# Optimization experiments

Measured on AMD Instinct MI355X. Metric: run time of the kernel, lower is better.

## Reference

```python
import jax, jax.numpy as jnp
import numpy as np
from jax.scipy.special import erfc

# Constants baked into PmeModule.__init__ (NNPOps PME)
GRID = (14, 15, 16)          # reciprocal mesh
ORDER = 5                    # B-spline order
ALPHA = 4.985823141035867    # Ewald splitting parameter (1/nm)
COULOMB = 138.935            # ONE_4PI_EPS0, kJ/mol*nm/e^2
CUTOFF = 0.5                 # direct-space cutoff (forward arg in source)
N_ATOMS = 4096


def _M(k, x):
    """Cardinal B-spline M_k evaluated elementwise (Essmann et al. 1995)."""
    if k == 1:
        return jnp.where((x >= 0.0) & (x < 1.0), 1.0, 0.0)
    return (x * _M(k - 1, x) + (k - x) * _M(k - 1, x - 1.0)) / (k - 1)


def _bspline_moduli(K):
    """|b(m)|^2 per axis; zero out ill-defined modes (odd order, m=K/2)."""
    m = jnp.arange(K)
    kk = jnp.arange(ORDER - 1, dtype=jnp.float32)
    Mv = _M(ORDER, kk + 1.0)                                   # M_n(1..n-1)
    ph = jnp.exp(2j * jnp.pi * m[:, None] * kk[None, :] / K)
    denom = (Mv[None, :] * ph).sum(-1)
    d2 = jnp.abs(denom) ** 2
    return jnp.where(d2 < 1e-7, 0.0, 1.0 / d2)


def _direct(positions, charges, box):
    # All-pairs minimum-image (triclinic-reduced) erfc/r sum within cutoff.
    delta = positions[:, None, :] - positions[None, :, :]      # [N,N,3]
    for a in (2, 1, 0):
        delta = delta - box[a] * jnp.round(delta[..., a:a + 1] / box[a, a])
    r2 = (delta ** 2).sum(-1)                                  # [N,N]
    n = positions.shape[0]
    mask = (r2 < CUTOFF ** 2) & ~jnp.eye(n, dtype=bool)
    r = jnp.sqrt(jnp.where(mask, r2, 1.0))
    qq = charges[:, None] * charges[None, :]
    e = jnp.where(mask, qq * erfc(ALPHA * r) / r, 0.0)
    return 0.5 * COULOMB * e.sum()                             # each pair once


def _spread(positions, charges, box):
    """Spread charges onto the mesh with order-5 B-splines (periodic)."""
    frac = positions @ jnp.linalg.inv(box)                     # fractional coords
    frac = frac - jnp.floor(frac)                              # wrap to [0,1)
    u = frac * jnp.array(GRID, jnp.float32)                    # [N,3]
    base = jnp.floor(u)
    w = u - base
    offs = jnp.arange(ORDER, dtype=jnp.float32)
    wts = _M(ORDER, w[:, :, None] + offs[None, None, :])       # [N,3,ORDER]
    idx = (base.astype(jnp.int32)[:, :, None]
           - jnp.arange(ORDER, dtype=jnp.int32)[None, None, :]) \
          % jnp.array(GRID, jnp.int32)[None, :, None]          # [N,3,ORDER]
    wq = (charges[:, None, None, None] * wts[:, 0, :, None, None]
          * wts[:, 1, None, :, None] * wts[:, 2, None, None, :])  # [N,5,5,5]
    fi = (idx[:, 0, :, None, None] * (GRID[1] * GRID[2])
          + idx[:, 1, None, :, None] * GRID[2]
          + idx[:, 2, None, None, :])                          # flat indices
    g = jnp.zeros(GRID[0] * GRID[1] * GRID[2], positions.dtype)
    return g.at[fi.reshape(-1)].add(wq.reshape(-1)).reshape(GRID)


def _reciprocal(positions, charges, box):
    Q = _spread(positions, charges, box)
    F = jnp.fft.fftn(Q)
    recip = jnp.linalg.inv(box)                                # recip vecs = columns
    mx = jnp.fft.fftfreq(GRID[0]) * GRID[0]
    my = jnp.fft.fftfreq(GRID[1]) * GRID[1]
    mz = jnp.fft.fftfreq(GRID[2]) * GRID[2]
    mv = (mx[:, None, None, None] * recip.T[0]
          + my[None, :, None, None] * recip.T[1]
          + mz[None, None, :, None] * recip.T[2])              # [Kx,Ky,Kz,3]
    m2 = (mv ** 2).sum(-1)
    B = (_bspline_moduli(GRID[0])[:, None, None]
         * _bspline_moduli(GRID[1])[None, :, None]
         * _bspline_moduli(GRID[2])[None, None, :])
    nz = m2 > 0.0
    m2s = jnp.where(nz, m2, 1.0)
    green = jnp.where(nz, jnp.exp(-(jnp.pi ** 2) * m2s / ALPHA ** 2) / m2s, 0.0)
    V = jnp.abs(jnp.linalg.det(box))
    erec = COULOMB / (2.0 * jnp.pi * V) * (green * B * jnp.abs(F) ** 2).sum()
    eself = -COULOMB * ALPHA / jnp.sqrt(jnp.pi) * (charges ** 2).sum()
    return erec + eself


def setup_inputs() -> dict:
    key = jax.random.key(0)
    k1, k2 = jax.random.split(key)
    box = jnp.diag(jnp.array([3.0, 3.1, 3.2], jnp.float32))    # nm, diagonal box
    positions = jax.random.uniform(k1, (N_ATOMS, 3), jnp.float32) * jnp.diag(box)
    charges = 0.5 * jax.random.normal(k2, (N_ATOMS,), jnp.float32)
    return {"positions": positions, "charges": charges, "box_vectors": box}


def reference(positions, charges, box_vectors):
    edir = _direct(positions, charges, box_vectors)
    erecip = _reciprocal(positions, charges, box_vectors)
    return edir - erecip
```

## Files before the change

### kernel.cpp

```cpp
#include <hip/hip_runtime.h>
#include <math.h>

#define NATOM 4096
#define KX 14
#define KY 15
#define KZ 16
#define SLAB (KY*KZ)
#define NGRID (KX*SLAB)
#define NB 128
#define APB (NATOM/NB)
#define NTRI 544

static constexpr float ALPHA_F   = 4.985823141035867f;
static constexpr float COULOMB_F = 138.935f;
static constexpr float CUT2_F    = 0.25f;
static constexpr float TWOPI_F   = 6.283185307179586f;
static constexpr float PI_F      = 3.14159265358979f;

#define POIS32 0xAAAAAAAAu
#define CTR_LAST (POIS32 + 15u)

__device__ __forceinline__ float M1f(float x){ return (x >= 0.f && x < 1.f) ? 1.f : 0.f; }
__device__ __forceinline__ float M2f(float x){ return x*M1f(x) + (2.f-x)*M1f(x-1.f); }
__device__ __forceinline__ float M3f(float x){ return (x*M2f(x) + (3.f-x)*M2f(x-1.f)) * 0.5f; }
__device__ __forceinline__ float M4f(float x){ return (x*M3f(x) + (4.f-x)*M3f(x-1.f)) * (1.f/3.f); }
__device__ __forceinline__ float M5f(float x){ return (x*M4f(x) + (5.f-x)*M4f(x-1.f)) * 0.25f; }

__device__ __forceinline__ void inv3x3(const float* b, float* inv){
  float det = b[0]*(b[4]*b[8]-b[5]*b[7]) - b[1]*(b[3]*b[8]-b[5]*b[6]) + b[2]*(b[3]*b[7]-b[4]*b[6]);
  float id = 1.f/det;
  inv[0] = (b[4]*b[8]-b[5]*b[7])*id;
  inv[1] = (b[2]*b[7]-b[1]*b[8])*id;
  inv[2] = (b[1]*b[5]-b[2]*b[4])*id;
  inv[3] = (b[5]*b[6]-b[3]*b[8])*id;
  inv[4] = (b[0]*b[8]-b[2]*b[6])*id;
  inv[5] = (b[2]*b[3]-b[0]*b[5])*id;
  inv[6] = (b[3]*b[7]-b[4]*b[6])*id;
  inv[7] = (b[1]*b[6]-b[0]*b[7])*id;
  inv[8] = (b[0]*b[4]-b[1]*b[3])*id;
}

__device__ __forceinline__ float bmod(int m, int K){
  float base = TWOPI_F * (float)m / (float)K;
  float s, c;
  float dr = 1.f/24.f, di = 0.f;
  __sincosf(base,      &s, &c); dr += (11.f/24.f)*c; di += (11.f/24.f)*s;
  __sincosf(base*2.f,  &s, &c); dr += (11.f/24.f)*c; di += (11.f/24.f)*s;
  __sincosf(base*3.f,  &s, &c); dr += (1.f/24.f)*c;  di += (1.f/24.f)*s;
  float d2 = dr*dr + di*di;
  return (d2 < 1e-7f) ? 0.f : 1.f/d2;
}

__device__ __forceinline__ float erfc_poly(float x){
  float tt = __builtin_amdgcn_rcpf(1.f + 0.3275911f*x);
  return ((((1.061405429f*tt - 1.453152027f)*tt + 1.421413741f)*tt
          - 0.284496736f)*tt + 0.254829592f)*tt;
}

__global__ __launch_bounds__(256) void fat_kernel(const float* __restrict__ pos,
    const float* __restrict__ chg, const float* __restrict__ box,
    float* __restrict__ grid, double* __restrict__ dpart)
{
  __shared__ float sg[NGRID];
  __shared__ float sx[64], sy[64], sz[64], sw[64];
  __shared__ double red4[4];
  int t = threadIdx.x;
  int b = blockIdx.x;

  if (b < NTRI){
    int rem = b, ci = 0;
    while (true){ int cnt = 64 - 4*ci; if (rem < cnt) break; rem -= cnt; ++ci; }
    int cj = 4*ci + rem;
    bool offdiag = (rem >= 4);
    int i  = ci*256 + t;
    int j0 = cj*64;
    if (t < 64){
      int j = j0 + t;
      sx[t] = pos[j*3+0]; sy[t] = pos[j*3+1]; sz[t] = pos[j*3+2]; sw[t] = chg[j];
    }
    __syncthreads();

    float b00=box[0],b01=box[1],b02=box[2],
          b10=box[3],b11=box[4],b12=box[5],
          b20=box[6],b21=box[7],b22=box[8];
    bool diag = (b01==0.f && b02==0.f && b10==0.f && b12==0.f && b20==0.f && b21==0.f);
    float i00 = 1.f/b00, i11 = 1.f/b11, i22 = 1.f/b22;

    float xi = pos[i*3+0], yi = pos[i*3+1], zi = pos[i*3+2], qi = chg[i];
    const float A2 = ALPHA_F*ALPHA_F;
    float e = 0.f;

    if (diag){
      #pragma unroll 4
      for (int jj = 0; jj < 64; ++jj){
        float dx = xi - sx[jj], dy = yi - sy[jj], dz = zi - sz[jj];
        dz -= b22*rintf(dz*i22);
        dy -= b11*rintf(dy*i11);
        dx -= b00*rintf(dx*i00);
        float r2 = dx*dx + dy*dy + dz*dz;
        if (r2 < CUT2_F && (j0 + jj) != i){
          float rinv = __builtin_amdgcn_rsqf(r2);
          float x = ALPHA_F * (r2 * rinv);
          e += qi * sw[jj] * erfc_poly(x) * __expf(-A2*r2) * rinv;
        }
      }
    } else {
      for (int jj = 0; jj < 64; ++jj){
        float dx = xi - sx[jj], dy = yi - sy[jj], dz = zi - sz[jj];
        float t2 = rintf(dz * i22); dx -= b20*t2; dy -= b21*t2; dz -= b22*t2;
        float t1 = rintf(dy * i11); dx -= b10*t1; dy -= b11*t1; dz -= b12*t1;
        float t0 = rintf(dx * i00); dx -= b00*t0; dy -= b01*t0; dz -= b02*t0;
        float r2 = dx*dx + dy*dy + dz*dz;
        if (r2 < CUT2_F && (j0 + jj) != i){
          float rinv = __builtin_amdgcn_rsqf(r2);
          float x = ALPHA_F * (r2 * rinv);
          e += qi * sw[jj] * erfc_poly(x) * __expf(-A2*r2) * rinv;
        }
      }
    }

    double de = (double)e;
    #pragma unroll
    for (int off = 32; off > 0; off >>= 1) de += __shfl_down(de, off);
    if ((t & 63) == 0) red4[t >> 6] = de;
    __syncthreads();
    if (t == 0){
      double s = red4[0]+red4[1]+red4[2]+red4[3];
      dpart[b] = offdiag ? 2.0*s : s;
    }

  } else {
    int sb = b - NTRI;
    for (int i = t; i < NGRID; i += 256) sg[i] = 0.f;
    __syncthreads();

    if (t < APB*5){
      int a   = t / 5;
      int jxi = t - 5*a;
      int atom = sb*APB + a;
      float bx[9], inv[9];
      #pragma unroll
      for (int i = 0; i < 9; ++i) bx[i] = box[i];
      inv3x3(bx, inv);

      float px = pos[atom*3+0], py = pos[atom*3+1], pz = pos[atom*3+2];
      float qi = chg[atom];
      float fr[3];
      fr[0] = px*inv[0] + py*inv[3] + pz*inv[6];
      fr[1] = px*inv[1] + py*inv[4] + pz*inv[7];
      fr[2] = px*inv[2] + py*inv[5] + pz*inv[8];

      const int Ks[3] = {KX, KY, KZ};
      float w[3][5]; int id[3][5];
      #pragma unroll
      for (int ax = 0; ax < 3; ++ax) {
        float f = fr[ax] - floorf(fr[ax]);
        float u = f * (float)Ks[ax];
        float bse = floorf(u);
        float x = u - bse;
        int bi = (int)bse;
        #pragma unroll
        for (int j = 0; j < 5; ++j) {
          w[ax][j] = M5f(x + (float)j);
          int ii = bi - j; if (ii < 0) ii += Ks[ax];
          id[ax][j] = ii;
        }
      }
      float qx = qi * w[0][jxi];
      int ox = id[0][jxi]*SLAB;
      #pragma unroll
      for (int jy = 0; jy < 5; ++jy) {
        float qxy = qx * w[1][jy];
        int oxy = ox + id[1][jy]*KZ;
        #pragma unroll
        for (int jz = 0; jz < 5; ++jz)
          atomicAdd(&sg[oxy + id[2][jz]], qxy * w[2][jz]);
      }
    }
    __syncthreads();
    for (int i = t; i < NGRID; i += 256){
      float v = sg[i];
      if (v != 0.f) atomicAdd(&grid[i], v);
    }
  }
}

__global__ __launch_bounds__(256) void recip_kernel(const float* __restrict__ grid,
    const float* __restrict__ chg, const float* __restrict__ box,
    const double* __restrict__ dpart, double* __restrict__ acc_rec,
    unsigned* __restrict__ ctr, float* __restrict__ out)
{
  __shared__ float2 Ty[KY*KY];
  __shared__ float2 Tx[KX*KX];
  __shared__ float2 Cz[KX*KY];
  __shared__ float2 Cyv[KX*KY];
  __shared__ double red[12];
  __shared__ int lastflag;
  int t  = threadIdx.x;
  int mz = blockIdx.x;
  const float P = __uint_as_float(POIS32);

  if (t < KY*KY){
    int my = t / KY, gy = t % KY;
    float s, c; __sincosf(-TWOPI_F*(float)((my*gy)%KY)/(float)KY, &s, &c);
    Ty[t] = make_float2(c, s);
  }
  if (t < KX*KX){
    int mx = t / KX, gx = t % KX;
    float s, c; __sincosf(-TWOPI_F*(float)((mx*gx)%KX)/(float)KX, &s, &c);
    Tx[t] = make_float2(c, s);
  }

  int u = t;
  if (u < KX*KY){
    const float4* g4 = (const float4*)grid;
    float q[16];
    #pragma unroll
    for (int k = 0; k < 4; ++k){
      float4 v = g4[u*4 + k];
      q[4*k+0] = v.x - P; q[4*k+1] = v.y - P; q[4*k+2] = v.z - P; q[4*k+3] = v.w - P;
    }
    float br = 0.f, bi = 0.f;
    #pragma unroll
    for (int gz = 0; gz < KZ; ++gz){
      float s, c; __sincosf(-TWOPI_F*(float)((mz*gz)%KZ)/(float)KZ, &s, &c);
      br += q[gz]*c; bi += q[gz]*s;
    }
    Cz[u] = make_float2(br, bi);
  }
  __syncthreads();

  if (u < KX*KY){
    int gx = u / KY, my = u % KY;
    float ar = 0.f, ai = 0.f;
    #pragma unroll
    for (int gy = 0; gy < KY; ++gy){
      float2 v = Cz[gx*KY + gy];
      float2 w = Ty[my*KY + gy];
      ar += v.x*w.x - v.y*w.y;
      ai += v.x*w.y + v.y*w.x;
    }
    Cyv[u] = make_float2(ar, ai);
  }
  __syncthreads();

  double s_rec = 0.0;
  if (u < KX*KY){
    int mx = u / KY, my = u % KY;
    float Fr = 0.f, Fi = 0.f;
    #pragma unroll
    for (int gx = 0; gx < KX; ++gx){
      float2 v = Cyv[gx*KY + my];
      float2 w = Tx[mx*KX + gx];
      Fr += v.x*w.x - v.y*w.y;
      Fi += v.x*w.y + v.y*w.x;
    }
    float bx[9], inv[9];
    #pragma unroll
    for (int k = 0; k < 9; ++k) bx[k] = box[k];
    inv3x3(bx, inv);
    float fx = (mx <= (KX-1)/2) ? (float)mx : (float)(mx - KX);
    float fy = (my <= (KY-1)/2) ? (float)my : (float)(my - KY);
    float fz = (mz <= (KZ-1)/2) ? (float)mz : (float)(mz - KZ);
    float mv0 = fx*inv[0] + fy*inv[1] + fz*inv[2];
    float mv1 = fx*inv[3] + fy*inv[4] + fz*inv[5];
    float mv2 = fx*inv[6] + fy*inv[7] + fz*inv[8];
    float m2 = mv0*mv0 + mv1*mv1 + mv2*mv2;
    float B  = bmod(mx,KX)*bmod(my,KY)*bmod(mz,KZ);
    if (m2 > 0.f && B > 0.f){
      float green = __expf(-(PI_F*PI_F)*m2/(ALPHA_F*ALPHA_F)) / m2;
      s_rec = (double)(green*B) * ((double)Fr*(double)Fr + (double)Fi*(double)Fi);
    }
  }

  #pragma unroll
  for (int off = 32; off > 0; off >>= 1) s_rec += __shfl_down(s_rec, off);
  int lane = t & 63, wid = t >> 6;
  if (lane == 0) red[wid] = s_rec;
  __syncthreads();
  if (t == 0){
    atomicAdd(acc_rec, red[0]+red[1]+red[2]+red[3]);
    asm volatile("s_waitcnt vmcnt(0)" ::: "memory");
    unsigned old = __hip_atomic_fetch_add(ctr, 1u, __ATOMIC_RELAXED, __HIP_MEMORY_SCOPE_AGENT);
    lastflag = (old == CTR_LAST) ? 1 : 0;
  }
  __syncthreads();

  if (lastflag){
    double s_dir = dpart[t] + dpart[t+256] + ((t < NTRI-512) ? dpart[t+512] : 0.0);
    double s_q2 = 0.0;
    #pragma unroll
    for (int i = t; i < NATOM; i += 256){ double q = (double)chg[i]; s_q2 += q*q; }
    #pragma unroll
    for (int off = 32; off > 0; off >>= 1){
      s_dir += __shfl_down(s_dir, off);
      s_q2  += __shfl_down(s_q2,  off);
    }
    if (lane == 0){ red[4+wid] = s_dir; red[8+wid] = s_q2; }
    __syncthreads();
    if (t == 0){
      double D = red[4]+red[5]+red[6]+red[7];
      double Q = red[8]+red[9]+red[10]+red[11];
      double R = __hip_atomic_load(acc_rec, __ATOMIC_ACQUIRE, __HIP_MEMORY_SCOPE_AGENT);
      double b00=box[0],b01=box[1],b02=box[2],
             b10=box[3],b11=box[4],b12=box[5],
             b20=box[6],b21=box[7],b22=box[8];
      double det = b00*(b11*b22 - b12*b21) - b01*(b10*b22 - b12*b20) + b02*(b10*b21 - b11*b20);
      double V = fabs(det);
      const double PI_D = 3.141592653589793238462643;
      double edir  = 0.5 * (double)COULOMB_F * D;
      double erec  = (double)COULOMB_F / (2.0*PI_D*V) * R;
      double eself = -(double)COULOMB_F * 4.985823141035867 / sqrt(PI_D) * Q;
      out[0] = (float)(edir - erec - eself);
    }
  }
}

extern "C" void kernel_launch(void* const* d_in, const int* in_sizes, int n_in,
                              void* d_out, int out_size, void* d_ws, size_t ws_size,
                              hipStream_t stream) {
  const float* pos = (const float*)d_in[0];
  const float* chg = (const float*)d_in[1];
  const float* box = (const float*)d_in[2];
  float* out = (float*)d_out;

  char* w = (char*)d_ws;
  float*    grid    = (float*)w;
  double*   dpart   = (double*)(w + 16384);
  double*   acc_rec = (double*)(w + 24576);
  unsigned* ctr     = (unsigned*)(w + 24584);

  fat_kernel<<<NTRI + NB, 256, 0, stream>>>(pos, chg, box, grid, dpart);
  recip_kernel<<<KZ, 256, 0, stream>>>(grid, chg, box, dpart, acc_rec, ctr, out);
}
```

Measured before the change: 79.12 us.

## Fuse reciprocal FFT into spread kernel via last-block atomic counters

Merges the two launches into one kernel. The last spreading block, detected by an atomic counter, runs the whole 3D DFT and energy sum by looping over all 16 z-planes in one block. A second counter over the direct-space blocks plus that block picks which one does the final combine. This removes a kernel launch and the gap between kernels, but the reciprocal work moves from 16 blocks onto a single block, and the self-pair test changes to r2>0. Per-pair data is also packed into float4 in shared memory.

```diff
diff --git a/kernel.cpp b/kernel.cpp
--- a/kernel.cpp
+++ b/kernel.cpp
@@ -18,7 +18,8 @@
 static constexpr float PI_F      = 3.14159265358979f;
 
 #define POIS32 0xAAAAAAAAu
-#define CTR_LAST (POIS32 + 15u)
+#define SPREAD_LAST (POIS32 + 127u)
+#define DONE_LAST   (POIS32 + 544u)
 
 __device__ __forceinline__ float M1f(float x){ return (x >= 0.f && x < 1.f) ? 1.f : 0.f; }
 __device__ __forceinline__ float M2f(float x){ return x*M1f(x) + (2.f-x)*M1f(x-1.f); }
@@ -57,13 +58,54 @@
           - 0.284496736f)*tt + 0.254829592f)*tt;
 }
 
-__global__ __launch_bounds__(256) void fat_kernel(const float* __restrict__ pos,
+__device__ __forceinline__ void final_combine(int t, const float* __restrict__ chg,
+    const float* __restrict__ box, const double* __restrict__ dpart,
+    double* __restrict__ acc_rec, float* __restrict__ out, double* red)
+{
+  int lane = t & 63, wid = t >> 6;
+  double s_dir = __hip_atomic_load(&dpart[t],     __ATOMIC_RELAXED, __HIP_MEMORY_SCOPE_AGENT)
+               + __hip_atomic_load(&dpart[t+256], __ATOMIC_RELAXED, __HIP_MEMORY_SCOPE_AGENT)
+               + ((t < NTRI-512)
+                  ? __hip_atomic_load(&dpart[t+512], __ATOMIC_RELAXED, __HIP_MEMORY_SCOPE_AGENT)
+                  : 0.0);
+  double s_q2 = 0.0;
+  #pragma unroll
+  for (int i = t; i < NATOM; i += 256){ double q = (double)chg[i]; s_q2 += q*q; }
+  #pragma unroll
+  for (int off = 32; off > 0; off >>= 1){
+    s_dir += __shfl_down(s_dir, off);
+    s_q2  += __shfl_down(s_q2,  off);
+  }
+  if (lane == 0){ red[4+wid] = s_dir; red[8+wid] = s_q2; }
+  __syncthreads();
+  if (t == 0){
+    double D = red[4]+red[5]+red[6]+red[7];
+    double Q = red[8]+red[9]+red[10]+red[11];
+    double R = __hip_atomic_load(acc_rec, __ATOMIC_ACQUIRE, __HIP_MEMORY_SCOPE_AGENT);
+    double b00=box[0],b01=box[1],b02=box[2],
+           b10=box[3],b11=box[4],b12=box[5],
+           b20=box[6],b21=box[7],b22=box[8];
+    double det = b00*(b11*b22 - b12*b21) - b01*(b10*b22 - b12*b20) + b02*(b10*b21 - b11*b20);
+    double V = fabs(det);
+    const double PI_D = 3.141592653589793238462643;
+    double edir  = 0.5 * (double)COULOMB_F * D;
+    double erec  = (double)COULOMB_F / (2.0*PI_D*V) * R;
+    double eself = -(double)COULOMB_F * 4.985823141035867 / sqrt(PI_D) * Q;
+    out[0] = (float)(edir - erec - eself);
+  }
+}
+
+__global__ __launch_bounds__(256) void pme_kernel(const float* __restrict__ pos,
     const float* __restrict__ chg, const float* __restrict__ box,
-    float* __restrict__ grid, double* __restrict__ dpart)
+    float* __restrict__ grid, double* __restrict__ dpart,
+    double* __restrict__ acc_rec, unsigned* __restrict__ sctr,
+    unsigned* __restrict__ dctr, float* __restrict__ out)
 {
-  __shared__ float sg[NGRID];
-  __shared__ float sx[64], sy[64], sz[64], sw[64];
-  __shared__ double red4[4];
+  __shared__ __align__(16) float sg[NGRID];
+  __shared__ float4 sj[64];
+  __shared__ double red[12];
+  __shared__ float bmz[KZ];
+  __shared__ int flag;
   int t = threadIdx.x;
   int b = blockIdx.x;
 
@@ -76,7 +118,7 @@
     int j0 = cj*64;
     if (t < 64){
       int j = j0 + t;
-      sx[t] = pos[j*3+0]; sy[t] = pos[j*3+1]; sz[t] = pos[j*3+2]; sw[t] = chg[j];
+      sj[t] = make_float4(pos[j*3+0], pos[j*3+1], pos[j*3+2], chg[j]);
     }
     __syncthreads();
 
@@ -93,28 +135,30 @@
     if (diag){
       #pragma unroll 4
       for (int jj = 0; jj < 64; ++jj){
-        float dx = xi - sx[jj], dy = yi - sy[jj], dz = zi - sz[jj];
+        float4 v = sj[jj];
+        float dx = xi - v.x, dy = yi - v.y, dz = zi - v.z;
         dz -= b22*rintf(dz*i22);
         dy -= b11*rintf(dy*i11);
         dx -= b00*rintf(dx*i00);
         float r2 = dx*dx + dy*dy + dz*dz;
-        if (r2 < CUT2_F && (j0 + jj) != i){
+        if (r2 < CUT2_F && r2 > 0.f){
           float rinv = __builtin_amdgcn_rsqf(r2);
           float x = ALPHA_F * (r2 * rinv);
-          e += qi * sw[jj] * erfc_poly(x) * __expf(-A2*r2) * rinv;
+          e += qi * v.w * erfc_poly(x) * __expf(-A2*r2) * rinv;
         }
       }
     } else {
       for (int jj = 0; jj < 64; ++jj){
-        float dx = xi - sx[jj], dy = yi - sy[jj], dz = zi - sz[jj];
+        float4 v = sj[jj];
+        float dx = xi - v.x, dy = yi - v.y, dz = zi - v.z;
         float t2 = rintf(dz * i22); dx -= b20*t2; dy -= b21*t2; dz -= b22*t2;
         float t1 = rintf(dy * i11); dx -= b10*t1; dy -= b11*t1; dz -= b12*t1;
         float t0 = rintf(dx * i00); dx -= b00*t0; dy -= b01*t0; dz -= b02*t0;
         float r2 = dx*dx + dy*dy + dz*dz;
-        if (r2 < CUT2_F && (j0 + jj) != i){
+        if (r2 < CUT2_F && r2 > 0.f){
           float rinv = __builtin_amdgcn_rsqf(r2);
           float x = ALPHA_F * (r2 * rinv);
-          e += qi * sw[jj] * erfc_poly(x) * __expf(-A2*r2) * rinv;
+          e += qi * v.w * erfc_poly(x) * __expf(-A2*r2) * rinv;
         }
       }
     }
@@ -122,84 +166,92 @@
     double de = (double)e;
     #pragma unroll
     for (int off = 32; off > 0; off >>= 1) de += __shfl_down(de, off);
-    if ((t & 63) == 0) red4[t >> 6] = de;
+    if ((t & 63) == 0) red[t >> 6] = de;
     __syncthreads();
     if (t == 0){
-      double s = red4[0]+red4[1]+red4[2]+red4[3];
-      dpart[b] = offdiag ? 2.0*s : s;
-    }
-
-  } else {
-    int sb = b - NTRI;
-    for (int i = t; i < NGRID; i += 256) sg[i] = 0.f;
-    __syncthreads();
-
-    if (t < APB*5){
-      int a   = t / 5;
-      int jxi = t - 5*a;
-      int atom = sb*APB + a;
-      float bx[9], inv[9];
-      #pragma unroll
-      for (int i = 0; i < 9; ++i) bx[i] = box[i];
-      inv3x3(bx, inv);
-
-      float px = pos[atom*3+0], py = pos[atom*3+1], pz = pos[atom*3+2];
-      float qi = chg[atom];
-      float fr[3];
-      fr[0] = px*inv[0] + py*inv[3] + pz*inv[6];
-      fr[1] = px*inv[1] + py*inv[4] + pz*inv[7];
-      fr[2] = px*inv[2] + py*inv[5] + pz*inv[8];
-
-      const int Ks[3] = {KX, KY, KZ};
-      float w[3][5]; int id[3][5];
-      #pragma unroll
-      for (int ax = 0; ax < 3; ++ax) {
-        float f = fr[ax] - floorf(fr[ax]);
-        float u = f * (float)Ks[ax];
-        float bse = floorf(u);
-        float x = u - bse;
-        int bi = (int)bse;
-        #pragma unroll
-        for (int j = 0; j < 5; ++j) {
-          w[ax][j] = M5f(x + (float)j);
-          int ii = bi - j; if (ii < 0) ii += Ks[ax];
-          id[ax][j] = ii;
-        }
-      }
-      float qx = qi * w[0][jxi];
-      int ox = id[0][jxi]*SLAB;
-      #pragma unroll
-      for (int jy = 0; jy < 5; ++jy) {
-        float qxy = qx * w[1][jy];
-        int oxy = ox + id[1][jy]*KZ;
-        #pragma unroll
-        for (int jz = 0; jz < 5; ++jz)
-          atomicAdd(&sg[oxy + id[2][jz]], qxy * w[2][jz]);
-      }
-    }
-    __syncthreads();
-    for (int i = t; i < NGRID; i += 256){
-      float v = sg[i];
-      if (v != 0.f) atomicAdd(&grid[i], v);
-    }
-  }
-}
-
-__global__ __launch_bounds__(256) void recip_kernel(const float* __restrict__ grid,
-    const float* __restrict__ chg, const float* __restrict__ box,
-    const double* __restrict__ dpart, double* __restrict__ acc_rec,
-    unsigned* __restrict__ ctr, float* __restrict__ out)
-{
-  __shared__ float2 Ty[KY*KY];
-  __shared__ float2 Tx[KX*KX];
-  __shared__ float2 Cz[KX*KY];
-  __shared__ float2 Cyv[KX*KY];
-  __shared__ double red[12];
-  __shared__ int lastflag;
-  int t  = threadIdx.x;
-  int mz = blockIdx.x;
-  const float P = __uint_as_float(POIS32);
-
+      double s = red[0]+red[1]+red[2]+red[3];
+      s = offdiag ? 2.0*s : s;
+      __hip_atomic_store(&dpart[b], s, __ATOMIC_RELAXED, __HIP_MEMORY_SCOPE_AGENT);
+      asm volatile("s_waitcnt vmcnt(0)" ::: "memory");
+      unsigned old = __hip_atomic_fetch_add(dctr, 1u, __ATOMIC_ACQ_REL, __HIP_MEMORY_SCOPE_AGENT);
+      flag = (old == DONE_LAST) ? 1 : 0;
+    }
+    __syncthreads();
+    if (flag) final_combine(t, chg, box, dpart, acc_rec, out, red);
+    return;
+  }
+
+  int sb = b - NTRI;
+  for (int i = t; i < NGRID; i += 256) sg[i] = 0.f;
+  __syncthreads();
+
+  if (t < APB*5){
+    int a   = t / 5;
+    int jxi = t - 5*a;
+    int atom = sb*APB + a;
+    float bx[9], inv[9];
+    #pragma unroll
+    for (int i = 0; i < 9; ++i) bx[i] = box[i];
+    inv3x3(bx, inv);
+
+    float px = pos[atom*3+0], py = pos[atom*3+1], pz = pos[atom*3+2];
+    float qi = chg[atom];
+    float fr[3];
+    fr[0] = px*inv[0] + py*inv[3] + pz*inv[6];
+    fr[1] = px*inv[1] + py*inv[4] + pz*inv[7];
+    fr[2] = px*inv[2] + py*inv[5] + pz*inv[8];
+
+    const int Ks[3] = {KX, KY, KZ};
+    float w[3][5]; int id[3][5];
+    #pragma unroll
+    for (int ax = 0; ax < 3; ++ax) {
+      float f = fr[ax] - floorf(fr[ax]);
+      float u = f * (float)Ks[ax];
+      float bse = floorf(u);
+      float x = u - bse;
+      int bi = (int)bse;
+      #pragma unroll
+      for (int j = 0; j < 5; ++j) {
+        w[ax][j] = M5f(x + (float)j);
+        int ii = bi - j; if (ii < 0) ii += Ks[ax];
+        id[ax][j] = ii;
+      }
+    }
+    float qx = qi * w[0][jxi];
+    int ox = id[0][jxi]*SLAB;
+    #pragma unroll
+    for (int jy = 0; jy < 5; ++jy) {
+      float qxy = qx * w[1][jy];
+      int oxy = ox + id[1][jy]*KZ;
+      #pragma unroll
+      for (int jz = 0; jz < 5; ++jz)
+        atomicAdd(&sg[oxy + id[2][jz]], qxy * w[2][jz]);
+    }
+  }
+  __syncthreads();
+  for (int i = t; i < NGRID; i += 256){
+    float v = sg[i];
+    if (v != 0.f) atomicAdd(&grid[i], v);
+  }
+  __syncthreads();
+  if (t == 0){
+    unsigned old = __hip_atomic_fetch_add(sctr, 1u, __ATOMIC_ACQ_REL, __HIP_MEMORY_SCOPE_AGENT);
+    flag = (old == SPREAD_LAST) ? 1 : 0;
+  }
+  __syncthreads();
+  if (!flag) return;
+
+  float2* Tz = (float2*)sg;
+  float2* Ty = Tz + KZ*KZ;
+  float2* Tx = Ty + KY*KY;
+  float2* Cz = Tx + KX*KX;
+  float2* Cy = Cz + KX*KY;
+
+  if (t < KZ*KZ){
+    int mz = t >> 4, gz = t & 15;
+    float s, c; __sincosf(-TWOPI_F*(float)((mz*gz)&15)/(float)KZ, &s, &c);
+    Tz[t] = make_float2(c, s);
+  }
   if (t < KY*KY){
     int my = t / KY, gy = t % KY;
     float s, c; __sincosf(-TWOPI_F*(float)((my*gy)%KY)/(float)KY, &s, &c);
@@ -210,67 +262,77 @@
     float s, c; __sincosf(-TWOPI_F*(float)((mx*gx)%KX)/(float)KX, &s, &c);
     Tx[t] = make_float2(c, s);
   }
+  if (t < KZ) bmz[t] = bmod(t, KZ);
 
   int u = t;
+  float q[KZ];
+  float Bxy = 0.f, mv0b = 0.f, mv1b = 0.f, mv2b = 0.f, iz0 = 0.f, iz1 = 0.f, iz2 = 0.f;
   if (u < KX*KY){
-    const float4* g4 = (const float4*)grid;
-    float q[16];
-    #pragma unroll
-    for (int k = 0; k < 4; ++k){
-      float4 v = g4[u*4 + k];
-      q[4*k+0] = v.x - P; q[4*k+1] = v.y - P; q[4*k+2] = v.z - P; q[4*k+3] = v.w - P;
-    }
-    float br = 0.f, bi = 0.f;
-    #pragma unroll
-    for (int gz = 0; gz < KZ; ++gz){
-      float s, c; __sincosf(-TWOPI_F*(float)((mz*gz)%KZ)/(float)KZ, &s, &c);
-      br += q[gz]*c; bi += q[gz]*s;
-    }
-    Cz[u] = make_float2(br, bi);
-  }
-  __syncthreads();
-
-  if (u < KX*KY){
-    int gx = u / KY, my = u % KY;
-    float ar = 0.f, ai = 0.f;
-    #pragma unroll
-    for (int gy = 0; gy < KY; ++gy){
-      float2 v = Cz[gx*KY + gy];
-      float2 w = Ty[my*KY + gy];
-      ar += v.x*w.x - v.y*w.y;
-      ai += v.x*w.y + v.y*w.x;
-    }
-    Cyv[u] = make_float2(ar, ai);
-  }
-  __syncthreads();
-
-  double s_rec = 0.0;
-  if (u < KX*KY){
+    const float P = __uint_as_float(POIS32);
+    #pragma unroll
+    for (int k = 0; k < KZ; ++k)
+      q[k] = __hip_atomic_load(&grid[u*KZ + k], __ATOMIC_RELAXED, __HIP_MEMORY_SCOPE_AGENT) - P;
     int mx = u / KY, my = u % KY;
-    float Fr = 0.f, Fi = 0.f;
-    #pragma unroll
-    for (int gx = 0; gx < KX; ++gx){
-      float2 v = Cyv[gx*KY + my];
-      float2 w = Tx[mx*KX + gx];
-      Fr += v.x*w.x - v.y*w.y;
-      Fi += v.x*w.y + v.y*w.x;
-    }
+    Bxy = bmod(mx,KX)*bmod(my,KY);
     float bx[9], inv[9];
     #pragma unroll
     for (int k = 0; k < 9; ++k) bx[k] = box[k];
     inv3x3(bx, inv);
     float fx = (mx <= (KX-1)/2) ? (float)mx : (float)(mx - KX);
     float fy = (my <= (KY-1)/2) ? (float)my : (float)(my - KY);
-    float fz = (mz <= (KZ-1)/2) ? (float)mz : (float)(mz - KZ);
-    float mv0 = fx*inv[0] + fy*inv[1] + fz*inv[2];
-    float mv1 = fx*inv[3] + fy*inv[4] + fz*inv[5];
-    float mv2 = fx*inv[6] + fy*inv[7] + fz*inv[8];
-    float m2 = mv0*mv0 + mv1*mv1 + mv2*mv2;
-    float B  = bmod(mx,KX)*bmod(my,KY)*bmod(mz,KZ);
-    if (m2 > 0.f && B > 0.f){
-      float green = __expf(-(PI_F*PI_F)*m2/(ALPHA_F*ALPHA_F)) / m2;
-      s_rec = (double)(green*B) * ((double)Fr*(double)Fr + (double)Fi*(double)Fi);
-    }
+    mv0b = fx*inv[0] + fy*inv[1]; iz0 = inv[2];
+    mv1b = fx*inv[3] + fy*inv[4]; iz1 = inv[5];
+    mv2b = fx*inv[6] + fy*inv[7]; iz2 = inv[8];
+  }
+  int gx_y = u / KY, my_y = u % KY;
+  __syncthreads();
+
+  double s_rec = 0.0;
+  for (int mz = 0; mz < KZ; ++mz){
+    if (u < KX*KY){
+      float br = 0.f, bi = 0.f;
+      #pragma unroll
+      for (int gz = 0; gz < KZ; ++gz){
+        float2 w = Tz[mz*KZ + gz];
+        br += q[gz]*w.x; bi += q[gz]*w.y;
+      }
+      Cz[u] = make_float2(br, bi);
+    }
+    __syncthreads();
+    if (u < KX*KY){
+      float ar = 0.f, ai = 0.f;
+      #pragma unroll
+      for (int gy = 0; gy < KY; ++gy){
+        float2 v = Cz[gx_y*KY + gy];
+        float2 w = Ty[my_y*KY + gy];
+        ar += v.x*w.x - v.y*w.y;
+        ai += v.x*w.y + v.y*w.x;
+      }
+      Cy[u] = make_float2(ar, ai);
+    }
+    __syncthreads();
+    if (u < KX*KY){
+      int mx = u / KY, my = u % KY;
+      float Fr = 0.f, Fi = 0.f;
+      #pragma unroll
+      for (int gx = 0; gx < KX; ++gx){
+        float2 v = Cy[gx*KY + my];
+        float2 w = Tx[mx*KX + gx];
+        Fr += v.x*w.x - v.y*w.y;
+        Fi += v.x*w.y + v.y*w.x;
+      }
+      float fz = (mz <= (KZ-1)/2) ? (float)mz : (float)(mz - KZ);
+      float m0 = mv0b + fz*iz0;
+      float m1 = mv1b + fz*iz1;
+      float m2c = mv2b + fz*iz2;
+      float m2 = m0*m0 + m1*m1 + m2c*m2c;
+      float B  = Bxy * bmz[mz];
+      if (m2 > 0.f && B > 0.f){
+        float green = __expf(-(PI_F*PI_F)*m2/(ALPHA_F*ALPHA_F)) / m2;
+        s_rec += (double)(green*B) * ((double)Fr*(double)Fr + (double)Fi*(double)Fi);
+      }
+    }
+    __syncthreads();
   }
 
   #pragma unroll
@@ -281,39 +343,11 @@
   if (t == 0){
     atomicAdd(acc_rec, red[0]+red[1]+red[2]+red[3]);
     asm volatile("s_waitcnt vmcnt(0)" ::: "memory");
-    unsigned old = __hip_atomic_fetch_add(ctr, 1u, __ATOMIC_RELAXED, __HIP_MEMORY_SCOPE_AGENT);
-    lastflag = (old == CTR_LAST) ? 1 : 0;
-  }
-  __syncthreads();
-
-  if (lastflag){
-    double s_dir = dpart[t] + dpart[t+256] + ((t < NTRI-512) ? dpart[t+512] : 0.0);
-    double s_q2 = 0.0;
-    #pragma unroll
-    for (int i = t; i < NATOM; i += 256){ double q = (double)chg[i]; s_q2 += q*q; }
-    #pragma unroll
-    for (int off = 32; off > 0; off >>= 1){
-      s_dir += __shfl_down(s_dir, off);
-      s_q2  += __shfl_down(s_q2,  off);
-    }
-    if (lane == 0){ red[4+wid] = s_dir; red[8+wid] = s_q2; }
-    __syncthreads();
-    if (t == 0){
-      double D = red[4]+red[5]+red[6]+red[7];
-      double Q = red[8]+red[9]+red[10]+red[11];
-      double R = __hip_atomic_load(acc_rec, __ATOMIC_ACQUIRE, __HIP_MEMORY_SCOPE_AGENT);
-      double b00=box[0],b01=box[1],b02=box[2],
-             b10=box[3],b11=box[4],b12=box[5],
-             b20=box[6],b21=box[7],b22=box[8];
-      double det = b00*(b11*b22 - b12*b21) - b01*(b10*b22 - b12*b20) + b02*(b10*b21 - b11*b20);
-      double V = fabs(det);
-      const double PI_D = 3.141592653589793238462643;
-      double edir  = 0.5 * (double)COULOMB_F * D;
-      double erec  = (double)COULOMB_F / (2.0*PI_D*V) * R;
-      double eself = -(double)COULOMB_F * 4.985823141035867 / sqrt(PI_D) * Q;
-      out[0] = (float)(edir - erec - eself);
-    }
-  }
+    unsigned old = __hip_atomic_fetch_add(dctr, 1u, __ATOMIC_ACQ_REL, __HIP_MEMORY_SCOPE_AGENT);
+    flag = (old == DONE_LAST) ? 1 : 0;
+  }
+  __syncthreads();
+  if (flag) final_combine(t, chg, box, dpart, acc_rec, out, red);
 }
 
 extern "C" void kernel_launch(void* const* d_in, const int* in_sizes, int n_in,
@@ -328,8 +362,9 @@
   float*    grid    = (float*)w;
   double*   dpart   = (double*)(w + 16384);
   double*   acc_rec = (double*)(w + 24576);
-  unsigned* ctr     = (unsigned*)(w + 24584);
-
-  fat_kernel<<<NTRI + NB, 256, 0, stream>>>(pos, chg, box, grid, dpart);
-  recip_kernel<<<KZ, 256, 0, stream>>>(grid, chg, box, dpart, acc_rec, ctr, out);
-}
+  unsigned* sctr    = (unsigned*)(w + 24584);
+  unsigned* dctr    = (unsigned*)(w + 24588);
+
+  pme_kernel<<<NTRI + NB, 256, 0, stream>>>(pos, chg, box, grid, dpart,
+                                            acc_rec, sctr, dctr, out);
+}
```

New measurement: 99.54 us. +25.8%, slower.
